# Performance work log

Measured on AMD Instinct MI355X. Metric: run time of the kernel, lower is better.

## Reference

```python
import jax, jax.numpy as jnp
import numpy as np

D_MODEL = 1024
NUM_HEADS = 16
D_HEAD = D_MODEL // NUM_HEADS


def setup_inputs() -> dict:
    key = jax.random.key(0)
    ks = jax.random.split(key, 11)
    B, S = 2, 2048
    s = 1.0 / np.sqrt(D_MODEL)
    inp = {
        "Q": jax.random.normal(ks[0], (B, S, D_MODEL), dtype=jnp.float32),
        "K": jax.random.normal(ks[1], (B, S, D_MODEL), dtype=jnp.float32),
        "V": jax.random.normal(ks[2], (B, S, D_MODEL), dtype=jnp.float32),
        "W_q": jax.random.normal(ks[3], (D_MODEL, D_MODEL), dtype=jnp.float32) * s,
        "b_q": jnp.zeros((D_MODEL,), dtype=jnp.float32),
        "W_k": jax.random.normal(ks[4], (D_MODEL, D_MODEL), dtype=jnp.float32) * s,
        "b_k": jnp.zeros((D_MODEL,), dtype=jnp.float32),
        "W_v": jax.random.normal(ks[5], (D_MODEL, D_MODEL), dtype=jnp.float32) * s,
        "b_v": jnp.zeros((D_MODEL,), dtype=jnp.float32),
        "W_o": jax.random.normal(ks[6], (D_MODEL, D_MODEL), dtype=jnp.float32) * s,
        "b_o": jnp.zeros((D_MODEL,), dtype=jnp.float32),
    }
    return inp


def reference(Q, K, V, W_q, b_q, W_k, b_k, W_v, b_v, W_o, b_o):
    B, S, _ = Q.shape
    # Linear projections (torch Linear: x @ W.T + b)
    q = Q @ W_q.T + b_q  # [B,S,D]
    k = K @ W_k.T + b_k
    v = V @ W_v.T + b_v
    # split heads -> [B,H,S,d]
    q = q.reshape(B, S, NUM_HEADS, D_HEAD).transpose(0, 2, 1, 3)
    k = k.reshape(B, S, NUM_HEADS, D_HEAD).transpose(0, 2, 1, 3)
    v = v.reshape(B, S, NUM_HEADS, D_HEAD).transpose(0, 2, 1, 3)
    scores = jnp.einsum("bhqd,bhkd->bhqk", q, k) / np.sqrt(D_HEAD).astype(np.float32)
    attn = jax.nn.softmax(scores, axis=-1)
    out = jnp.einsum("bhqk,bhkd->bhqd", attn, v)
    out = out.transpose(0, 2, 1, 3).reshape(B, S, D_MODEL)
    return out @ W_o.T + b_o
```

## Files before the change

kernel.cpp:

```cpp
#include <hip/hip_runtime.h>
#include <stdint.h>

#define D_MODEL 1024
#define S_LEN   2048
#define BATCH   2
#define NHEAD   16
#define DHEAD   64
#define NTOK    (BATCH * S_LEN)

typedef unsigned short u16;
typedef __attribute__((ext_vector_type(8))) short bf16x8;
typedef __attribute__((ext_vector_type(4))) float f32x4;
typedef __attribute__((ext_vector_type(16))) float f32x16;
typedef __attribute__((ext_vector_type(2))) unsigned int u32x2;

__device__ __forceinline__ unsigned pack2bf(float lo, float hi) {
    unsigned a = __float_as_uint(lo) + 0x8000u;
    unsigned b = __float_as_uint(hi) + 0x8000u;
    return __builtin_amdgcn_perm(b, a, 0x07060302u);
}
__device__ __forceinline__ u16 f2bf1(float f) {
    return (u16)((__float_as_uint(f) + 0x8000u) >> 16);
}

#define GAS(p) ((const __attribute__((address_space(1))) void*)(p))
#define LAS(p) ((__attribute__((address_space(3))) void*)(p))
#define SWZ8(row, c) (((((row) << 3) | ((c) ^ ((row) & 7)))) << 3)

__global__ __launch_bounds__(256) void convert_kernel(
    const float* __restrict__ Q, const float* __restrict__ K, const float* __restrict__ V,
    const float* __restrict__ Wq, const float* __restrict__ Wk,
    const float* __restrict__ Wv, const float* __restrict__ Wo,
    u16* __restrict__ Qb, u16* __restrict__ Kb, u16* __restrict__ Vb,
    u16* __restrict__ Wqb, u16* __restrict__ Wkb, u16* __restrict__ Wvb, u16* __restrict__ Wob)
{
    const size_t SEG = 262144;
    size_t start = (size_t)blockIdx.x * 4096;
    int s = (int)(start / SEG);
    const float* src; u16* dst; size_t seg0;
    if (s < 4)       { src = Q;  dst = Qb;  seg0 = 0; }
    else if (s < 8)  { src = K;  dst = Kb;  seg0 = 4 * SEG; }
    else if (s < 12) { src = V;  dst = Vb;  seg0 = 8 * SEG; }
    else if (s == 12){ src = Wq; dst = Wqb; seg0 = 12 * SEG; }
    else if (s == 13){ src = Wk; dst = Wkb; seg0 = 13 * SEG; }
    else if (s == 14){ src = Wv; dst = Wvb; seg0 = 14 * SEG; }
    else             { src = Wo; dst = Wob; seg0 = 15 * SEG; }
    size_t off = start - seg0 + threadIdx.x;
    const float4* s4 = (const float4*)src;
    #pragma unroll
    for (int k = 0; k < 16; ++k) {
        float4 x = s4[off + (size_t)k * 256];
        u32x2 p = (u32x2){pack2bf(x.x, x.y), pack2bf(x.z, x.w)};
        *(u32x2*)(dst + (off + (size_t)k * 256) * 4) = p;
    }
}

__global__ __launch_bounds__(512, 2) void proj_kernel(
    const u16* __restrict__ Qb, const u16* __restrict__ Kb, const u16* __restrict__ Vb,
    const u16* __restrict__ Wqb, const u16* __restrict__ Wkb, const u16* __restrict__ Wvb,
    const float* __restrict__ bq, const float* __restrict__ bk, const float* __restrict__ bv,
    u16* __restrict__ qw, u16* __restrict__ kw, u16* __restrict__ vtw)
{
    const int bid = blockIdx.x;
    const int wid = (bid & 7) * 24 + (bid >> 3);
    const int z = wid >> 6;
    const int r = wid & 63;
    const int nbase = (r >> 2) * 256;
    const int mbase = (r & 3) * 256;

    const u16* Ag = (z == 0) ? Wqb : (z == 1) ? Wkb : Wvb;
    const u16* Bg = (z == 0) ? Qb  : (z == 1) ? Kb  : Vb;
    const float* bias = (z == 0) ? bq : (z == 1) ? bk : bv;

    const int tid = threadIdx.x, lane = tid & 63, wave = tid >> 6;
    const int l31 = lane & 31, hh = lane >> 5;
    const int wm = wave >> 2;
    const int wn = wave & 3;

    __shared__ __align__(16) u16 smem[65536];

    size_t aoff[4], boff[4];
    #pragma unroll
    for (int c = 0; c < 4; ++c) {
        int p = (wave * 4 + c) * 64 + lane;
        int row = p >> 3;
        int cg  = (p & 7) ^ (row & 7);
        aoff[c] = (size_t)(mbase + row) * D_MODEL + cg * 8;
        boff[c] = (size_t)(nbase + row) * D_MODEL + cg * 8;
    }

#define STAGE(buf, kc)                                                              \
    do {                                                                            \
        _Pragma("unroll")                                                           \
        for (int c = 0; c < 4; ++c) {                                               \
            __builtin_amdgcn_global_load_lds(GAS(Ag + aoff[c] + (kc)),              \
                LAS(smem + (buf) * 16384 + (wave * 4 + c) * 512), 16, 0, 0);        \
            __builtin_amdgcn_global_load_lds(GAS(Bg + boff[c] + (kc)),              \
                LAS(smem + 32768 + (buf) * 16384 + (wave * 4 + c) * 512), 16, 0, 0);\
        }                                                                           \
    } while (0)

    STAGE(0, 0);

    f32x16 acc[4][2];
    #pragma unroll
    for (int mt = 0; mt < 4; ++mt)
        #pragma unroll
        for (int nt = 0; nt < 2; ++nt)
            #pragma unroll
            for (int q = 0; q < 16; ++q) acc[mt][nt][q] = 0.f;

    for (int t = 0; t < D_MODEL / 64; ++t) {
        const int cur = t & 1;
        asm volatile("s_waitcnt vmcnt(0) lgkmcnt(0)" ::: "memory");
        __builtin_amdgcn_s_barrier();
        asm volatile("" ::: "memory");
        if (t < D_MODEL / 64 - 1) STAGE(cur ^ 1, (t + 1) * 64);
        const u16* Ab = smem + cur * 16384;
        const u16* Bb = smem + 32768 + cur * 16384;
        #pragma unroll
        for (int kk = 0; kk < 4; ++kk) {
            bf16x8 af[4], bfr[2];
            #pragma unroll
            for (int mt = 0; mt < 4; ++mt)
                af[mt] = *(const bf16x8*)&Ab[SWZ8(wm * 128 + mt * 32 + l31, kk * 2 + hh)];
            #pragma unroll
            for (int nt = 0; nt < 2; ++nt)
                bfr[nt] = *(const bf16x8*)&Bb[SWZ8(wn * 64 + nt * 32 + l31, kk * 2 + hh)];
            #pragma unroll
            for (int mt = 0; mt < 4; ++mt)
                #pragma unroll
                for (int nt = 0; nt < 2; ++nt)
                    acc[mt][nt] = __builtin_amdgcn_mfma_f32_32x32x16_bf16(af[mt], bfr[nt], acc[mt][nt], 0, 0, 0);
        }
    }
#undef STAGE

    if (z < 2) {
        u16* Y = z ? kw : qw;
        const float scale = z ? 1.0f : 0.18033688011112042f;
        #pragma unroll
        for (int mt = 0; mt < 4; ++mt)
            #pragma unroll
            for (int nt = 0; nt < 2; ++nt) {
                const int tok = nbase + wn * 64 + nt * 32 + l31;
                u16* yrow = Y + (size_t)tok * D_MODEL;
                #pragma unroll
                for (int g = 0; g < 4; ++g) {
                    const int d0 = mbase + wm * 128 + mt * 32 + 8 * g + 4 * hh;
                    float4 b4 = *(const float4*)&bias[d0];
                    float v0 = (acc[mt][nt][4 * g + 0] + b4.x) * scale;
                    float v1 = (acc[mt][nt][4 * g + 1] + b4.y) * scale;
                    float v2 = (acc[mt][nt][4 * g + 2] + b4.z) * scale;
                    float v3 = (acc[mt][nt][4 * g + 3] + b4.w) * scale;
                    *(u32x2*)(yrow + d0) = (u32x2){pack2bf(v0, v1), pack2bf(v2, v3)};
                }
            }
    } else {
        #pragma unroll
        for (int mt = 0; mt < 4; ++mt)
            #pragma unroll
            for (int nt = 0; nt < 2; ++nt) {
                const int tok = nbase + wn * 64 + nt * 32 + l31;
                #pragma unroll
                for (int g = 0; g < 4; ++g) {
                    const int d0 = mbase + wm * 128 + mt * 32 + 8 * g + 4 * hh;
                    #pragma unroll
                    for (int q = 0; q < 4; ++q)
                        vtw[(size_t)(d0 + q) * NTOK + tok] =
                            f2bf1(acc[mt][nt][4 * g + q] + bias[d0 + q]);
                }
            }
    }
}

__global__ __launch_bounds__(512, 2) void attn_kernel(
    const u16* __restrict__ qw, const u16* __restrict__ kw,
    const u16* __restrict__ vtw, u16* __restrict__ aw)
{
    const int bid = blockIdx.x;
    const int w = (bid & 7) * 32 + (bid >> 3);
    const int qbase = (w & 7) * 256;
    const int g = w >> 3;
    const int h = g & 15, b = g >> 4;

    const int tid = threadIdx.x, lane = tid & 63, wave = tid >> 6;
    const int wq = wave & 3;
    const int wk = wave >> 2;
    const int l31 = lane & 31;
    const int hh  = lane >> 5;
    const int colbase = h * DHEAD;
    const size_t qrow0 = (size_t)b * S_LEN + qbase;

    __shared__ __align__(16) u16 smem[35328];
    #define KS_OFF(buf) ((buf) * 4096)
    #define VS_OFF(buf) (8192 + (buf) * 4096)

    const int srow = tid >> 3;
    const int scg  = (tid & 7) ^ (srow & 7);
    const size_t ksrc = ((size_t)b * S_LEN + srow) * D_MODEL + colbase + scg * 8;
    const size_t vsrc = (size_t)(colbase + srow) * NTOK + (size_t)b * S_LEN + scg * 8;

    #define STAGE_KV(buf, kv0)                                                         \
        do {                                                                           \
            __builtin_amdgcn_global_load_lds(GAS(kw + ksrc + (size_t)(kv0) * D_MODEL), \
                                             LAS(smem + KS_OFF(buf) + wave * 512), 16, 0, 0); \
            __builtin_amdgcn_global_load_lds(GAS(vtw + vsrc + (kv0)),                  \
                                             LAS(smem + VS_OFF(buf) + wave * 512), 16, 0, 0); \
        } while (0)

    bf16x8 qf0[4], qf1[4];
    {
        const u16* qp0 = qw + (qrow0 + wq * 64 + l31) * D_MODEL + colbase + hh * 8;
        const u16* qp1 = qw + (qrow0 + wq * 64 + 32 + l31) * D_MODEL + colbase + hh * 8;
        #pragma unroll
        for (int s = 0; s < 4; ++s) {
            qf0[s] = *(const bf16x8*)(qp0 + s * 16);
            qf1[s] = *(const bf16x8*)(qp1 + s * 16);
        }
    }

    STAGE_KV(0, 0);

    f32x16 o0[2], o1[2];
    #pragma unroll
    for (int dt = 0; dt < 2; ++dt)
        #pragma unroll
        for (int r = 0; r < 16; ++r) { o0[dt][r] = 0.f; o1[dt][r] = 0.f; }
    float l0 = 0.f, l1 = 0.f;

    __syncthreads();

    for (int t = 0; t < S_LEN / 64; ++t) {
        const int cur = t & 1;
        if (t + 1 < S_LEN / 64) STAGE_KV(!cur, (t + 1) * 64);

        f32x16 sc0, sc1;
        #pragma unroll
        for (int r = 0; r < 16; ++r) { sc0[r] = -12.f; sc1[r] = -12.f; }
        __builtin_amdgcn_s_setprio(1);
        #pragma unroll
        for (int s = 0; s < 4; ++s) {
            bf16x8 kf = *(const bf16x8*)&smem[KS_OFF(cur) + SWZ8(wk * 32 + l31, s * 2 + hh)];
            sc0 = __builtin_amdgcn_mfma_f32_32x32x16_bf16(kf, qf0[s], sc0, 0, 0, 0);
            sc1 = __builtin_amdgcn_mfma_f32_32x32x16_bf16(kf, qf1[s], sc1, 0, 0, 0);
        }
        __builtin_amdgcn_s_setprio(0);

        unsigned x0[4][2], x1[4][2];
        #pragma unroll
        for (int gg = 0; gg < 4; ++gg) {
            float p0 = __builtin_amdgcn_exp2f(sc0[4 * gg + 0]);
            float p1 = __builtin_amdgcn_exp2f(sc0[4 * gg + 1]);
            float p2 = __builtin_amdgcn_exp2f(sc0[4 * gg + 2]);
            float p3 = __builtin_amdgcn_exp2f(sc0[4 * gg + 3]);
            l0 += (p0 + p1) + (p2 + p3);
            asm("v_cvt_pk_bf16_f32 %0, %1, %2" : "=v"(x0[gg][0]) : "v"(p0), "v"(p1));
            asm("v_cvt_pk_bf16_f32 %0, %1, %2" : "=v"(x0[gg][1]) : "v"(p2), "v"(p3));
            float q0 = __builtin_amdgcn_exp2f(sc1[4 * gg + 0]);
            float q1 = __builtin_amdgcn_exp2f(sc1[4 * gg + 1]);
            float q2 = __builtin_amdgcn_exp2f(sc1[4 * gg + 2]);
            float q3 = __builtin_amdgcn_exp2f(sc1[4 * gg + 3]);
            l1 += (q0 + q1) + (q2 + q3);
            asm("v_cvt_pk_bf16_f32 %0, %1, %2" : "=v"(x1[gg][0]) : "v"(q0), "v"(q1));
            asm("v_cvt_pk_bf16_f32 %0, %1, %2" : "=v"(x1[gg][1]) : "v"(q2), "v"(q3));
        }

        #pragma unroll
        for (int sp = 0; sp < 2; ++sp) {
            unsigned a0 = x0[2 * sp][0], b0 = x0[2 * sp + 1][0];
            unsigned a1 = x0[2 * sp][1], b1 = x0[2 * sp + 1][1];
            asm("v_permlane32_swap_b32 %0, %1" : "+v"(a0), "+v"(b0));
            asm("v_permlane32_swap_b32 %0, %1" : "+v"(a1), "+v"(b1));
            union { unsigned u[4]; bf16x8 v; } pf0;
            pf0.u[0] = a0; pf0.u[1] = a1; pf0.u[2] = b0; pf0.u[3] = b1;
            unsigned c0 = x1[2 * sp][0], d0 = x1[2 * sp + 1][0];
            unsigned c1 = x1[2 * sp][1], d1 = x1[2 * sp + 1][1];
            asm("v_permlane32_swap_b32 %0, %1" : "+v"(c0), "+v"(d0));
            asm("v_permlane32_swap_b32 %0, %1" : "+v"(c1), "+v"(d1));
            union { unsigned u[4]; bf16x8 v; } pf1;
            pf1.u[0] = c0; pf1.u[1] = c1; pf1.u[2] = d0; pf1.u[3] = d1;
            __builtin_amdgcn_s_setprio(1);
            #pragma unroll
            for (int dt = 0; dt < 2; ++dt) {
                bf16x8 vf = *(const bf16x8*)&smem[VS_OFF(cur) + SWZ8(dt * 32 + l31, wk * 4 + sp * 2 + hh)];
                o0[dt] = __builtin_amdgcn_mfma_f32_32x32x16_bf16(vf, pf0.v, o0[dt], 0, 0, 0);
                o1[dt] = __builtin_amdgcn_mfma_f32_32x32x16_bf16(vf, pf1.v, o1[dt], 0, 0, 0);
            }
            __builtin_amdgcn_s_setprio(0);
        }

        __syncthreads();
    }

    l0 += __shfl_xor(l0, 32);
    l1 += __shfl_xor(l1, 32);

    float* Ored = (float*)smem;
    float* Lred = (float*)(smem + 34816);
    float* op0 = Ored + ((size_t)wq * 64 + l31) * 68;
    float* op1 = Ored + ((size_t)wq * 64 + 32 + l31) * 68;
    if (wk == 1) {
        #pragma unroll
        for (int dt = 0; dt < 2; ++dt)
            #pragma unroll
            for (int gg = 0; gg < 4; ++gg) {
                *(f32x4*)(op0 + dt * 32 + 8 * gg + 4 * hh) =
                    (f32x4){o0[dt][4 * gg + 0], o0[dt][4 * gg + 1], o0[dt][4 * gg + 2], o0[dt][4 * gg + 3]};
                *(f32x4*)(op1 + dt * 32 + 8 * gg + 4 * hh) =
                    (f32x4){o1[dt][4 * gg + 0], o1[dt][4 * gg + 1], o1[dt][4 * gg + 2], o1[dt][4 * gg + 3]};
            }
        if (hh == 0) {
            Lred[wq * 64 + l31] = l0;
            Lred[wq * 64 + 32 + l31] = l1;
        }
    }
    __syncthreads();
    if (wk == 0) {
        l0 += Lred[wq * 64 + l31];
        l1 += Lred[wq * 64 + 32 + l31];
        float inv0 = 1.0f / l0, inv1 = 1.0f / l1;
        size_t orow0 = (qrow0 + wq * 64 + l31) * D_MODEL + colbase;
        size_t orow1 = (qrow0 + wq * 64 + 32 + l31) * D_MODEL + colbase;
        #pragma unroll
        for (int dt = 0; dt < 2; ++dt)
            #pragma unroll
            for (int gg = 0; gg < 4; ++gg) {
                f32x4 add0 = *(const f32x4*)(op0 + dt * 32 + 8 * gg + 4 * hh);
                f32x4 add1 = *(const f32x4*)(op1 + dt * 32 + 8 * gg + 4 * hh);
                float v0 = (o0[dt][4 * gg + 0] + add0[0]) * inv0;
                float v1 = (o0[dt][4 * gg + 1] + add0[1]) * inv0;
                float v2 = (o0[dt][4 * gg + 2] + add0[2]) * inv0;
                float v3 = (o0[dt][4 * gg + 3] + add0[3]) * inv0;
                *(u32x2*)(aw + orow0 + dt * 32 + 8 * gg + 4 * hh) =
                    (u32x2){pack2bf(v0, v1), pack2bf(v2, v3)};
                float u0 = (o1[dt][4 * gg + 0] + add1[0]) * inv1;
                float u1 = (o1[dt][4 * gg + 1] + add1[1]) * inv1;
                float u2 = (o1[dt][4 * gg + 2] + add1[2]) * inv1;
                float u3 = (o1[dt][4 * gg + 3] + add1[3]) * inv1;
                *(u32x2*)(aw + orow1 + dt * 32 + 8 * gg + 4 * hh) =
                    (u32x2){pack2bf(u0, u1), pack2bf(u2, u3)};
            }
    }
    #undef STAGE_KV
    #undef KS_OFF
    #undef VS_OFF
}

__global__ __launch_bounds__(512, 2) void outproj_kernel(
    const u16* __restrict__ aw, const u16* __restrict__ Wob,
    const float* __restrict__ bo, float* __restrict__ out)
{
    const int bid = blockIdx.x;
    const int wid = (bid & 7) * 32 + (bid >> 3);
    const int mbase = (wid & 7) * 128;
    const int nbase = (wid >> 3) * 128;

    const int tid = threadIdx.x, lane = tid & 63, wave = tid >> 6;
    const int l31 = lane & 31, hh = lane >> 5;
    const int wm = wave >> 2;
    const int wn = wave & 3;

    __shared__ __align__(16) u16 smem[32768];

    size_t aoff[2], boff[2];
    #pragma unroll
    for (int c = 0; c < 2; ++c) {
        int p = c * 512 + tid;
        int row = p >> 3;
        int cg  = (p & 7) ^ (row & 7);
        aoff[c] = (size_t)(mbase + row) * D_MODEL + cg * 8;
        boff[c] = (size_t)(nbase + row) * D_MODEL + cg * 8;
    }

#define OSTAGE(buf, kc)                                                             \
    do {                                                                            \
        _Pragma("unroll")                                                           \
        for (int c = 0; c < 2; ++c) {                                               \
            __builtin_amdgcn_global_load_lds(GAS(Wob + aoff[c] + (kc)),             \
                LAS(smem + (buf) * 8192 + c * 4096 + wave * 512), 16, 0, 0);        \
            __builtin_amdgcn_global_load_lds(GAS(aw + boff[c] + (kc)),              \
                LAS(smem + 16384 + (buf) * 8192 + c * 4096 + wave * 512), 16, 0, 0);\
        }                                                                           \
    } while (0)

    OSTAGE(0, 0);

    f32x16 acc[2];
    #pragma unroll
    for (int mt = 0; mt < 2; ++mt)
        #pragma unroll
        for (int q = 0; q < 16; ++q) acc[mt][q] = 0.f;

    for (int t = 0; t < D_MODEL / 64; ++t) {
        const int cur = t & 1;
        asm volatile("s_waitcnt vmcnt(0) lgkmcnt(0)" ::: "memory");
        __builtin_amdgcn_s_barrier();
        asm volatile("" ::: "memory");
        if (t < D_MODEL / 64 - 1) OSTAGE(cur ^ 1, (t + 1) * 64);
        const u16* Ab = smem + cur * 8192;
        const u16* Bb = smem + 16384 + cur * 8192;
        #pragma unroll
        for (int kk = 0; kk < 4; ++kk) {
            bf16x8 af[2], bfr;
            #pragma unroll
            for (int mt = 0; mt < 2; ++mt)
                af[mt] = *(const bf16x8*)&Ab[SWZ8(wm * 64 + mt * 32 + l31, kk * 2 + hh)];
            bfr = *(const bf16x8*)&Bb[SWZ8(wn * 32 + l31, kk * 2 + hh)];
            __builtin_amdgcn_s_setprio(1);
            #pragma unroll
            for (int mt = 0; mt < 2; ++mt)
                acc[mt] = __builtin_amdgcn_mfma_f32_32x32x16_bf16(af[mt], bfr, acc[mt], 0, 0, 0);
            __builtin_amdgcn_s_setprio(0);
        }
    }
#undef OSTAGE

    const int tok = nbase + wn * 32 + l31;
    float* orow = out + (size_t)tok * D_MODEL;
    #pragma unroll
    for (int mt = 0; mt < 2; ++mt)
        #pragma unroll
        for (int g = 0; g < 4; ++g) {
            const int d0 = mbase + wm * 64 + mt * 32 + 8 * g + 4 * hh;
            float4 b4 = *(const float4*)&bo[d0];
            float4 st;
            st.x = acc[mt][4 * g + 0] + b4.x;
            st.y = acc[mt][4 * g + 1] + b4.y;
            st.z = acc[mt][4 * g + 2] + b4.z;
            st.w = acc[mt][4 * g + 3] + b4.w;
            *(float4*)(orow + d0) = st;
        }
}

extern "C" void kernel_launch(void* const* d_in, const int* in_sizes, int n_in,
                              void* d_out, int out_size, void* d_ws, size_t ws_size,
                              hipStream_t stream) {
    const float* Q  = (const float*)d_in[0];
    const float* K  = (const float*)d_in[1];
    const float* V  = (const float*)d_in[2];
    const float* Wq = (const float*)d_in[3];
    const float* bq = (const float*)d_in[4];
    const float* Wk = (const float*)d_in[5];
    const float* bk = (const float*)d_in[6];
    const float* Wv = (const float*)d_in[7];
    const float* bv = (const float*)d_in[8];
    const float* Wo = (const float*)d_in[9];
    const float* bo = (const float*)d_in[10];

    const size_t NT = (size_t)NTOK * D_MODEL;
    const size_t WN = (size_t)D_MODEL * D_MODEL;
    u16* base = (u16*)d_ws;
    u16* qw  = base;
    u16* kw  = base + NT;
    u16* vtw = base + 2 * NT;
    u16* Qb  = base + 3 * NT;
    u16* Kb  = base + 4 * NT;
    u16* Vb  = base + 5 * NT;
    u16* Wqb = base + 6 * NT;
    u16* Wkb = Wqb + WN;
    u16* Wvb = Wkb + WN;
    u16* Wob = Wvb + WN;
    u16* aww = Qb;

    convert_kernel<<<1024, 256, 0, stream>>>(Q, K, V, Wq, Wk, Wv, Wo,
                                             Qb, Kb, Vb, Wqb, Wkb, Wvb, Wob);
    proj_kernel<<<dim3(192), 512, 0, stream>>>(Qb, Kb, Vb, Wqb, Wkb, Wvb,
                                               bq, bk, bv, qw, kw, vtw);
    attn_kernel<<<dim3(256), 512, 0, stream>>>(qw, kw, vtw, aww);
    outproj_kernel<<<dim3(256), 512, 0, stream>>>(aww, Wob, bo, (float*)d_out);
}
```

Measured before the change: 210.6 us.

## Fuse fp32-to-bf16 conversion into projection GEMM staging, drop convert kernel

Removes the separate conversion kernel. The QKV projection and output projection kernels now load fp32 inputs and weights into registers, pack them to bf16, and write them swizzled into LDS. This replaces the direct global_load_lds path with a register-staged prefetch that overlaps with the MFMA loop. It saves a full pass over the inputs and the bf16 workspace, but doubles global read bytes per tile inside the GEMMs and adds VGPR pressure and LDS write instructions.

Result: slower. 235.4 us (+11.8%).

```diff
diff --git a/kernel.cpp b/kernel.cpp
--- a/kernel.cpp
+++ b/kernel.cpp
@@ -13,6 +13,7 @@
 typedef __attribute__((ext_vector_type(4))) float f32x4;
 typedef __attribute__((ext_vector_type(16))) float f32x16;
 typedef __attribute__((ext_vector_type(2))) unsigned int u32x2;
+typedef __attribute__((ext_vector_type(4))) unsigned int u32x4;
 
 __device__ __forceinline__ unsigned pack2bf(float lo, float hi) {
     unsigned a = __float_as_uint(lo) + 0x8000u;
@@ -27,37 +28,9 @@
 #define LAS(p) ((__attribute__((address_space(3))) void*)(p))
 #define SWZ8(row, c) (((((row) << 3) | ((c) ^ ((row) & 7)))) << 3)
 
-__global__ __launch_bounds__(256) void convert_kernel(
+__global__ __launch_bounds__(512, 2) void proj_kernel(
     const float* __restrict__ Q, const float* __restrict__ K, const float* __restrict__ V,
-    const float* __restrict__ Wq, const float* __restrict__ Wk,
-    const float* __restrict__ Wv, const float* __restrict__ Wo,
-    u16* __restrict__ Qb, u16* __restrict__ Kb, u16* __restrict__ Vb,
-    u16* __restrict__ Wqb, u16* __restrict__ Wkb, u16* __restrict__ Wvb, u16* __restrict__ Wob)
-{
-    const size_t SEG = 262144;
-    size_t start = (size_t)blockIdx.x * 4096;
-    int s = (int)(start / SEG);
-    const float* src; u16* dst; size_t seg0;
-    if (s < 4)       { src = Q;  dst = Qb;  seg0 = 0; }
-    else if (s < 8)  { src = K;  dst = Kb;  seg0 = 4 * SEG; }
-    else if (s < 12) { src = V;  dst = Vb;  seg0 = 8 * SEG; }
-    else if (s == 12){ src = Wq; dst = Wqb; seg0 = 12 * SEG; }
-    else if (s == 13){ src = Wk; dst = Wkb; seg0 = 13 * SEG; }
-    else if (s == 14){ src = Wv; dst = Wvb; seg0 = 14 * SEG; }
-    else             { src = Wo; dst = Wob; seg0 = 15 * SEG; }
-    size_t off = start - seg0 + threadIdx.x;
-    const float4* s4 = (const float4*)src;
-    #pragma unroll
-    for (int k = 0; k < 16; ++k) {
-        float4 x = s4[off + (size_t)k * 256];
-        u32x2 p = (u32x2){pack2bf(x.x, x.y), pack2bf(x.z, x.w)};
-        *(u32x2*)(dst + (off + (size_t)k * 256) * 4) = p;
-    }
-}
-
-__global__ __launch_bounds__(512, 2) void proj_kernel(
-    const u16* __restrict__ Qb, const u16* __restrict__ Kb, const u16* __restrict__ Vb,
-    const u16* __restrict__ Wqb, const u16* __restrict__ Wkb, const u16* __restrict__ Wvb,
+    const float* __restrict__ Wq, const float* __restrict__ Wk, const float* __restrict__ Wv,
     const float* __restrict__ bq, const float* __restrict__ bk, const float* __restrict__ bv,
     u16* __restrict__ qw, u16* __restrict__ kw, u16* __restrict__ vtw)
 {
@@ -68,8 +41,8 @@
     const int nbase = (r >> 2) * 256;
     const int mbase = (r & 3) * 256;
 
-    const u16* Ag = (z == 0) ? Wqb : (z == 1) ? Wkb : Wvb;
-    const u16* Bg = (z == 0) ? Qb  : (z == 1) ? Kb  : Vb;
+    const float* Ag = (z == 0) ? Wq : (z == 1) ? Wk : Wv;
+    const float* Bg = (z == 0) ? Q  : (z == 1) ? K  : V;
     const float* bias = (z == 0) ? bq : (z == 1) ? bk : bv;
 
     const int tid = threadIdx.x, lane = tid & 63, wave = tid >> 6;
@@ -79,28 +52,53 @@
 
     __shared__ __align__(16) u16 smem[65536];
 
+    int srow[4], scol[4];
     size_t aoff[4], boff[4];
     #pragma unroll
     for (int c = 0; c < 4; ++c) {
-        int p = (wave * 4 + c) * 64 + lane;
-        int row = p >> 3;
-        int cg  = (p & 7) ^ (row & 7);
-        aoff[c] = (size_t)(mbase + row) * D_MODEL + cg * 8;
-        boff[c] = (size_t)(nbase + row) * D_MODEL + cg * 8;
-    }
-
-#define STAGE(buf, kc)                                                              \
-    do {                                                                            \
-        _Pragma("unroll")                                                           \
-        for (int c = 0; c < 4; ++c) {                                               \
-            __builtin_amdgcn_global_load_lds(GAS(Ag + aoff[c] + (kc)),              \
-                LAS(smem + (buf) * 16384 + (wave * 4 + c) * 512), 16, 0, 0);        \
-            __builtin_amdgcn_global_load_lds(GAS(Bg + boff[c] + (kc)),              \
-                LAS(smem + 32768 + (buf) * 16384 + (wave * 4 + c) * 512), 16, 0, 0);\
-        }                                                                           \
+        int p = c * 512 + tid;
+        srow[c] = p >> 3;
+        scol[c] = p & 7;
+        aoff[c] = (size_t)(mbase + srow[c]) * D_MODEL + scol[c] * 8;
+        boff[c] = (size_t)(nbase + srow[c]) * D_MODEL + scol[c] * 8;
+    }
+
+    float4 ar[4][2], br[4][2];
+
+#define PISSUE(kc)                                                          \
+    do {                                                                    \
+        _Pragma("unroll")                                                   \
+        for (int c = 0; c < 4; ++c) {                                       \
+            const float4* ap = (const float4*)(Ag + aoff[c] + (kc));        \
+            const float4* bp = (const float4*)(Bg + boff[c] + (kc));        \
+            ar[c][0] = ap[0]; ar[c][1] = ap[1];                             \
+            br[c][0] = bp[0]; br[c][1] = bp[1];                             \
+        }                                                                   \
     } while (0)
 
-    STAGE(0, 0);
+#define PWRITE(buf)                                                         \
+    do {                                                                    \
+        _Pragma("unroll")                                                   \
+        for (int c = 0; c < 4; ++c) {                                       \
+            u32x4 wa, wb;                                                   \
+            wa[0] = pack2bf(ar[c][0].x, ar[c][0].y);                        \
+            wa[1] = pack2bf(ar[c][0].z, ar[c][0].w);                        \
+            wa[2] = pack2bf(ar[c][1].x, ar[c][1].y);                        \
+            wa[3] = pack2bf(ar[c][1].z, ar[c][1].w);                        \
+            wb[0] = pack2bf(br[c][0].x, br[c][0].y);                        \
+            wb[1] = pack2bf(br[c][0].z, br[c][0].w);                        \
+            wb[2] = pack2bf(br[c][1].x, br[c][1].y);                        \
+            wb[3] = pack2bf(br[c][1].z, br[c][1].w);                        \
+            *(u32x4*)&smem[(buf) * 16384 + SWZ8(srow[c], scol[c])] = wa;    \
+            *(u32x4*)&smem[32768 + (buf) * 16384 + SWZ8(srow[c], scol[c])] = wb; \
+        }                                                                   \
+    } while (0)
+
+    PISSUE(0);
+    PWRITE(0);
+    asm volatile("s_waitcnt lgkmcnt(0)" ::: "memory");
+    __builtin_amdgcn_s_barrier();
+    asm volatile("" ::: "memory");
 
     f32x16 acc[4][2];
     #pragma unroll
@@ -112,10 +110,7 @@
 
     for (int t = 0; t < D_MODEL / 64; ++t) {
         const int cur = t & 1;
-        asm volatile("s_waitcnt vmcnt(0) lgkmcnt(0)" ::: "memory");
-        __builtin_amdgcn_s_barrier();
-        asm volatile("" ::: "memory");
-        if (t < D_MODEL / 64 - 1) STAGE(cur ^ 1, (t + 1) * 64);
+        if (t < D_MODEL / 64 - 1) PISSUE((t + 1) * 64);
         const u16* Ab = smem + cur * 16384;
         const u16* Bb = smem + 32768 + cur * 16384;
         #pragma unroll
@@ -133,8 +128,13 @@
                 for (int nt = 0; nt < 2; ++nt)
                     acc[mt][nt] = __builtin_amdgcn_mfma_f32_32x32x16_bf16(af[mt], bfr[nt], acc[mt][nt], 0, 0, 0);
         }
-    }
-#undef STAGE
+        if (t < D_MODEL / 64 - 1) PWRITE(cur ^ 1);
+        asm volatile("s_waitcnt lgkmcnt(0)" ::: "memory");
+        __builtin_amdgcn_s_barrier();
+        asm volatile("" ::: "memory");
+    }
+#undef PISSUE
+#undef PWRITE
 
     if (z < 2) {
         u16* Y = z ? kw : qw;
@@ -348,7 +348,7 @@
 }
 
 __global__ __launch_bounds__(512, 2) void outproj_kernel(
-    const u16* __restrict__ aw, const u16* __restrict__ Wob,
+    const u16* __restrict__ aw, const float* __restrict__ Wo,
     const float* __restrict__ bo, float* __restrict__ out)
 {
     const int bid = blockIdx.x;
@@ -363,28 +363,63 @@
 
     __shared__ __align__(16) u16 smem[32768];
 
-    size_t aoff[2], boff[2];
+    int arow[2], acol[2];
+    size_t aoff[2];
     #pragma unroll
     for (int c = 0; c < 2; ++c) {
         int p = c * 512 + tid;
-        int row = p >> 3;
-        int cg  = (p & 7) ^ (row & 7);
-        aoff[c] = (size_t)(mbase + row) * D_MODEL + cg * 8;
-        boff[c] = (size_t)(nbase + row) * D_MODEL + cg * 8;
-    }
-
-#define OSTAGE(buf, kc)                                                             \
-    do {                                                                            \
-        _Pragma("unroll")                                                           \
-        for (int c = 0; c < 2; ++c) {                                               \
-            __builtin_amdgcn_global_load_lds(GAS(Wob + aoff[c] + (kc)),             \
-                LAS(smem + (buf) * 8192 + c * 4096 + wave * 512), 16, 0, 0);        \
-            __builtin_amdgcn_global_load_lds(GAS(aw + boff[c] + (kc)),              \
-                LAS(smem + 16384 + (buf) * 8192 + c * 4096 + wave * 512), 16, 0, 0);\
-        }                                                                           \
+        arow[c] = p >> 3;
+        acol[c] = p & 7;
+        aoff[c] = (size_t)(mbase + arow[c]) * D_MODEL + acol[c] * 8;
+    }
+    int brow[2], bcg[2];
+    size_t boff[2];
+    #pragma unroll
+    for (int c = 0; c < 2; ++c) {
+        int p = c * 512 + tid;
+        brow[c] = p >> 3;
+        bcg[c]  = (p & 7) ^ (brow[c] & 7);
+        boff[c] = (size_t)(nbase + brow[c]) * D_MODEL + bcg[c] * 8;
+    }
+
+    float4 wr[2][2];
+
+#define OISSUE_A(kc)                                                        \
+    do {                                                                    \
+        _Pragma("unroll")                                                   \
+        for (int c = 0; c < 2; ++c) {                                       \
+            const float4* ap = (const float4*)(Wo + aoff[c] + (kc));        \
+            wr[c][0] = ap[0]; wr[c][1] = ap[1];                             \
+        }                                                                   \
     } while (0)
 
-    OSTAGE(0, 0);
+#define OWRITE_A(buf)                                                       \
+    do {                                                                    \
+        _Pragma("unroll")                                                   \
+        for (int c = 0; c < 2; ++c) {                                       \
+            u32x4 wa;                                                       \
+            wa[0] = pack2bf(wr[c][0].x, wr[c][0].y);                        \
+            wa[1] = pack2bf(wr[c][0].z, wr[c][0].w);                        \
+            wa[2] = pack2bf(wr[c][1].x, wr[c][1].y);                        \
+            wa[3] = pack2bf(wr[c][1].z, wr[c][1].w);                        \
+            *(u32x4*)&smem[(buf) * 8192 + SWZ8(arow[c], acol[c])] = wa;     \
+        }                                                                   \
+    } while (0)
+
+#define OSTAGE_B(buf, kc)                                                   \
+    do {                                                                    \
+        _Pragma("unroll")                                                   \
+        for (int c = 0; c < 2; ++c)                                         \
+            __builtin_amdgcn_global_load_lds(GAS(aw + boff[c] + (kc)),      \
+                LAS(smem + 16384 + (buf) * 8192 + c * 4096 + tid * 8), 16, 0, 0); \
+    } while (0)
+
+    OISSUE_A(0);
+    OSTAGE_B(0, 0);
+    OWRITE_A(0);
+    asm volatile("s_waitcnt vmcnt(0) lgkmcnt(0)" ::: "memory");
+    __builtin_amdgcn_s_barrier();
+    asm volatile("" ::: "memory");
 
     f32x16 acc[2];
     #pragma unroll
@@ -394,10 +429,10 @@
 
     for (int t = 0; t < D_MODEL / 64; ++t) {
         const int cur = t & 1;
-        asm volatile("s_waitcnt vmcnt(0) lgkmcnt(0)" ::: "memory");
-        __builtin_amdgcn_s_barrier();
-        asm volatile("" ::: "memory");
-        if (t < D_MODEL / 64 - 1) OSTAGE(cur ^ 1, (t + 1) * 64);
+        if (t < D_MODEL / 64 - 1) {
+            OISSUE_A((t + 1) * 64);
+            OSTAGE_B(cur ^ 1, (t + 1) * 64);
+        }
         const u16* Ab = smem + cur * 8192;
         const u16* Bb = smem + 16384 + cur * 8192;
         #pragma unroll
@@ -413,8 +448,14 @@
                 acc[mt] = __builtin_amdgcn_mfma_f32_32x32x16_bf16(af[mt], bfr, acc[mt], 0, 0, 0);
             __builtin_amdgcn_s_setprio(0);
         }
-    }
-#undef OSTAGE
+        if (t < D_MODEL / 64 - 1) OWRITE_A(cur ^ 1);
+        asm volatile("s_waitcnt vmcnt(0) lgkmcnt(0)" ::: "memory");
+        __builtin_amdgcn_s_barrier();
+        asm volatile("" ::: "memory");
+    }
+#undef OISSUE_A
+#undef OWRITE_A
+#undef OSTAGE_B
 
     const int tok = nbase + wn * 32 + l31;
     float* orow = out + (size_t)tok * D_MODEL;
@@ -449,24 +490,14 @@
     const float* bo = (const float*)d_in[10];
 
     const size_t NT = (size_t)NTOK * D_MODEL;
-    const size_t WN = (size_t)D_MODEL * D_MODEL;
     u16* base = (u16*)d_ws;
     u16* qw  = base;
     u16* kw  = base + NT;
     u16* vtw = base + 2 * NT;
-    u16* Qb  = base + 3 * NT;
-    u16* Kb  = base + 4 * NT;
-    u16* Vb  = base + 5 * NT;
-    u16* Wqb = base + 6 * NT;
-    u16* Wkb = Wqb + WN;
-    u16* Wvb = Wkb + WN;
-    u16* Wob = Wvb + WN;
-    u16* aww = Qb;
-
-    convert_kernel<<<1024, 256, 0, stream>>>(Q, K, V, Wq, Wk, Wv, Wo,
-                                             Qb, Kb, Vb, Wqb, Wkb, Wvb, Wob);
-    proj_kernel<<<dim3(192), 512, 0, stream>>>(Qb, Kb, Vb, Wqb, Wkb, Wvb,
+    u16* aww = base + 3 * NT;
+
+    proj_kernel<<<dim3(192), 512, 0, stream>>>(Q, K, V, Wq, Wk, Wv,
                                                bq, bk, bv, qw, kw, vtw);
     attn_kernel<<<dim3(256), 512, 0, stream>>>(qw, kw, vtw, aww);
-    outproj_kernel<<<dim3(256), 512, 0, stream>>>(aww, Wob, bo, (float*)d_out);
+    outproj_kernel<<<dim3(256), 512, 0, stream>>>(aww, Wo, bo, (float*)d_out);
 }
```

## Restructure QKV projection GEMM into phased pipeline with per-wave token strips

Applied to the files above, without the earlier changes.

Reorganises the QKV projection GEMM so each wave owns a 32-token strip across all 256 output features, instead of a 128x64 sub-tile. Each K step is split into four phases, with partial vmcnt waits and barriers between them. Next-tile global-to-LDS loads are issued in chunks interleaved with MFMA work, and setprio raises priority around the MFMA bursts. The aim is to overlap memory latency with compute rather than draining all loads each iteration. The cost is more barriers per step and a different LDS read pattern, with more A-fragment reads per wave.

Result: no change. 214.3 us (+1.8%).

```diff
diff --git a/kernel.cpp b/kernel.cpp
--- a/kernel.cpp
+++ b/kernel.cpp
@@ -74,102 +74,117 @@
 
     const int tid = threadIdx.x, lane = tid & 63, wave = tid >> 6;
     const int l31 = lane & 31, hh = lane >> 5;
-    const int wm = wave >> 2;
-    const int wn = wave & 3;
 
     __shared__ __align__(16) u16 smem[65536];
 
-    size_t aoff[4], boff[4];
-    #pragma unroll
-    for (int c = 0; c < 4; ++c) {
-        int p = (wave * 4 + c) * 64 + lane;
-        int row = p >> 3;
-        int cg  = (p & 7) ^ (row & 7);
-        aoff[c] = (size_t)(mbase + row) * D_MODEL + cg * 8;
-        boff[c] = (size_t)(nbase + row) * D_MODEL + cg * 8;
-    }
-
-#define STAGE(buf, kc)                                                              \
-    do {                                                                            \
-        _Pragma("unroll")                                                           \
-        for (int c = 0; c < 4; ++c) {                                               \
-            __builtin_amdgcn_global_load_lds(GAS(Ag + aoff[c] + (kc)),              \
-                LAS(smem + (buf) * 16384 + (wave * 4 + c) * 512), 16, 0, 0);        \
-            __builtin_amdgcn_global_load_lds(GAS(Bg + boff[c] + (kc)),              \
-                LAS(smem + 32768 + (buf) * 16384 + (wave * 4 + c) * 512), 16, 0, 0);\
-        }                                                                           \
+    const int srow = tid >> 3;
+    const int scg  = (tid & 7) ^ (srow & 7);
+    const size_t abase = (size_t)(mbase + srow) * D_MODEL + scg * 8;
+    const size_t bbase = (size_t)(nbase + srow) * D_MODEL + scg * 8;
+
+#define STG_A(pp, c, kc) __builtin_amdgcn_global_load_lds(                     \
+        GAS(Ag + abase + (size_t)(c) * 65536 + (kc)),                          \
+        LAS(smem + (pp) * 16384 + (c) * 4096 + tid * 8), 16, 0, 0)
+#define STG_B(pp, c, kc) __builtin_amdgcn_global_load_lds(                     \
+        GAS(Bg + bbase + (size_t)(c) * 65536 + (kc)),                          \
+        LAS(smem + 32768 + (pp) * 16384 + (c) * 4096 + tid * 8), 16, 0, 0)
+
+    STG_B(0, 0, 0); STG_B(0, 1, 0); STG_B(0, 2, 0); STG_B(0, 3, 0);
+    STG_A(0, 0, 0); STG_A(0, 1, 0); STG_A(0, 2, 0); STG_A(0, 3, 0);
+
+    f32x16 acc[8];
+    #pragma unroll
+    for (int m = 0; m < 8; ++m)
+        #pragma unroll
+        for (int q = 0; q < 16; ++q) acc[m][q] = 0.f;
+
+    const int bchunk = wave >> 1;
+    const int brow   = (wave & 1) * 32 + l31;
+
+#define PH_MFMA(q, AcP)                                                          \
+    do {                                                                         \
+        const u16* Ac = (AcP);                                                   \
+        bf16x8 a0[4], a1[4];                                                     \
+        _Pragma("unroll")                                                        \
+        for (int kk = 0; kk < 4; ++kk) {                                         \
+            a0[kk] = *(const bf16x8*)&Ac[SWZ8(l31, kk * 2 + hh)];                \
+            a1[kk] = *(const bf16x8*)&Ac[SWZ8(32 + l31, kk * 2 + hh)];           \
+        }                                                                        \
+        __builtin_amdgcn_s_setprio(1);                                           \
+        _Pragma("unroll")                                                        \
+        for (int kk = 0; kk < 4; ++kk) {                                         \
+            acc[2 * (q)]     = __builtin_amdgcn_mfma_f32_32x32x16_bf16(a0[kk], bf[kk], acc[2 * (q)], 0, 0, 0);     \
+            acc[2 * (q) + 1] = __builtin_amdgcn_mfma_f32_32x32x16_bf16(a1[kk], bf[kk], acc[2 * (q) + 1], 0, 0, 0); \
+        }                                                                        \
+        __builtin_amdgcn_s_setprio(0);                                           \
     } while (0)
 
-    STAGE(0, 0);
-
-    f32x16 acc[4][2];
-    #pragma unroll
-    for (int mt = 0; mt < 4; ++mt)
-        #pragma unroll
-        for (int nt = 0; nt < 2; ++nt)
-            #pragma unroll
-            for (int q = 0; q < 16; ++q) acc[mt][nt][q] = 0.f;
-
-    for (int t = 0; t < D_MODEL / 64; ++t) {
-        const int cur = t & 1;
-        asm volatile("s_waitcnt vmcnt(0) lgkmcnt(0)" ::: "memory");
+    for (int t = 0; t < 16; ++t) {
+        const int p = t & 1, np = p ^ 1;
+        const int kc1 = (t + 1) * 64;
+        const u16* Abase = smem + p * 16384;
+        const u16* Bc = smem + 32768 + p * 16384 + bchunk * 4096;
+        bf16x8 bf[4];
+
+        if (t < 15) { asm volatile("s_waitcnt vmcnt(2)" ::: "memory"); }
+        else        { asm volatile("s_waitcnt vmcnt(0)" ::: "memory"); }
         __builtin_amdgcn_s_barrier();
         asm volatile("" ::: "memory");
-        if (t < D_MODEL / 64 - 1) STAGE(cur ^ 1, (t + 1) * 64);
-        const u16* Ab = smem + cur * 16384;
-        const u16* Bb = smem + 32768 + cur * 16384;
-        #pragma unroll
-        for (int kk = 0; kk < 4; ++kk) {
-            bf16x8 af[4], bfr[2];
-            #pragma unroll
-            for (int mt = 0; mt < 4; ++mt)
-                af[mt] = *(const bf16x8*)&Ab[SWZ8(wm * 128 + mt * 32 + l31, kk * 2 + hh)];
-            #pragma unroll
-            for (int nt = 0; nt < 2; ++nt)
-                bfr[nt] = *(const bf16x8*)&Bb[SWZ8(wn * 64 + nt * 32 + l31, kk * 2 + hh)];
-            #pragma unroll
-            for (int mt = 0; mt < 4; ++mt)
-                #pragma unroll
-                for (int nt = 0; nt < 2; ++nt)
-                    acc[mt][nt] = __builtin_amdgcn_mfma_f32_32x32x16_bf16(af[mt], bfr[nt], acc[mt][nt], 0, 0, 0);
-        }
-    }
-#undef STAGE
-
+        if (t < 15) { STG_B(np, 0, kc1); STG_B(np, 1, kc1); }
+        #pragma unroll
+        for (int kk = 0; kk < 4; ++kk)
+            bf[kk] = *(const bf16x8*)&Bc[SWZ8(brow, kk * 2 + hh)];
+        PH_MFMA(0, Abase + 0 * 4096);
+
+        if (t < 15) { asm volatile("s_waitcnt vmcnt(4)" ::: "memory"); }
+        __builtin_amdgcn_s_barrier();
+        asm volatile("" ::: "memory");
+        if (t < 15) { STG_B(np, 2, kc1); STG_B(np, 3, kc1); }
+        PH_MFMA(1, Abase + 1 * 4096);
+
+        if (t < 15) { asm volatile("s_waitcnt vmcnt(4)" ::: "memory"); }
+        __builtin_amdgcn_s_barrier();
+        asm volatile("" ::: "memory");
+        if (t < 15) { STG_A(np, 0, kc1); STG_A(np, 1, kc1); }
+        PH_MFMA(2, Abase + 2 * 4096);
+
+        if (t < 15) { asm volatile("s_waitcnt vmcnt(6)" ::: "memory"); }
+        __builtin_amdgcn_s_barrier();
+        asm volatile("" ::: "memory");
+        if (t < 15) { STG_A(np, 2, kc1); STG_A(np, 3, kc1); }
+        PH_MFMA(3, Abase + 3 * 4096);
+    }
+#undef PH_MFMA
+#undef STG_A
+#undef STG_B
+
+    const int tok = nbase + wave * 32 + l31;
     if (z < 2) {
         u16* Y = z ? kw : qw;
         const float scale = z ? 1.0f : 0.18033688011112042f;
-        #pragma unroll
-        for (int mt = 0; mt < 4; ++mt)
-            #pragma unroll
-            for (int nt = 0; nt < 2; ++nt) {
-                const int tok = nbase + wn * 64 + nt * 32 + l31;
-                u16* yrow = Y + (size_t)tok * D_MODEL;
-                #pragma unroll
-                for (int g = 0; g < 4; ++g) {
-                    const int d0 = mbase + wm * 128 + mt * 32 + 8 * g + 4 * hh;
-                    float4 b4 = *(const float4*)&bias[d0];
-                    float v0 = (acc[mt][nt][4 * g + 0] + b4.x) * scale;
-                    float v1 = (acc[mt][nt][4 * g + 1] + b4.y) * scale;
-                    float v2 = (acc[mt][nt][4 * g + 2] + b4.z) * scale;
-                    float v3 = (acc[mt][nt][4 * g + 3] + b4.w) * scale;
-                    *(u32x2*)(yrow + d0) = (u32x2){pack2bf(v0, v1), pack2bf(v2, v3)};
-                }
+        u16* yrow = Y + (size_t)tok * D_MODEL;
+        #pragma unroll
+        for (int m = 0; m < 8; ++m)
+            #pragma unroll
+            for (int g = 0; g < 4; ++g) {
+                const int d0 = mbase + m * 32 + 8 * g + 4 * hh;
+                float4 b4 = *(const float4*)&bias[d0];
+                float v0 = (acc[m][4 * g + 0] + b4.x) * scale;
+                float v1 = (acc[m][4 * g + 1] + b4.y) * scale;
+                float v2 = (acc[m][4 * g + 2] + b4.z) * scale;
+                float v3 = (acc[m][4 * g + 3] + b4.w) * scale;
+                *(u32x2*)(yrow + d0) = (u32x2){pack2bf(v0, v1), pack2bf(v2, v3)};
             }
     } else {
         #pragma unroll
-        for (int mt = 0; mt < 4; ++mt)
-            #pragma unroll
-            for (int nt = 0; nt < 2; ++nt) {
-                const int tok = nbase + wn * 64 + nt * 32 + l31;
+        for (int m = 0; m < 8; ++m)
+            #pragma unroll
+            for (int g = 0; g < 4; ++g) {
+                const int d0 = mbase + m * 32 + 8 * g + 4 * hh;
                 #pragma unroll
-                for (int g = 0; g < 4; ++g) {
-                    const int d0 = mbase + wm * 128 + mt * 32 + 8 * g + 4 * hh;
-                    #pragma unroll
-                    for (int q = 0; q < 4; ++q)
-                        vtw[(size_t)(d0 + q) * NTOK + tok] =
-                            f2bf1(acc[mt][nt][4 * g + q] + bias[d0 + q]);
-                }
+                for (int q = 0; q < 4; ++q)
+                    vtw[(size_t)(d0 + q) * NTOK + tok] =
+                        f2bf1(acc[m][4 * g + q] + bias[d0 + q]);
             }
     }
 }
```
